# Performance work log

Hardware: AMD Instinct MI355X
Metric: run time of the kernel (lower is better)

The kernel has to match this reference:

```python
import jax, jax.numpy as jnp
import numpy as np

T, B, E, H = 2048, 2, 1024, 16
HD = E // H
EPS = 1e-5


def setup_inputs() -> dict:
    key = jax.random.key(0)
    k1, k2, k3 = jax.random.split(key, 3)
    bound_in = float(np.sqrt(6.0 / (3 * E + E)))   # xavier_uniform for [3E,E]
    bound_out = float(np.sqrt(6.0 / (E + E)))      # xavier_uniform for [E,E]
    return {
        "query": jax.random.normal(k1, (T, B, E), dtype=jnp.float32),
        "gamma": jnp.ones((E,), dtype=jnp.float32),
        "beta": jnp.zeros((E,), dtype=jnp.float32),
        "in_proj_weight": jax.random.uniform(k2, (3 * E, E), jnp.float32, -bound_in, bound_in),
        "out_proj_weight": jax.random.uniform(k3, (E, E), jnp.float32, -bound_out, bound_out),
    }


def reference(query, gamma, beta, in_proj_weight, out_proj_weight):
    # LayerNorm over channel dim
    mean = jnp.mean(query, axis=-1, keepdims=True)
    var = jnp.mean(jnp.square(query - mean), axis=-1, keepdims=True)
    ln = (query - mean) * jax.lax.rsqrt(var + EPS) * gamma + beta  # [T,B,E]

    # Fused QKV projection (no bias): qkv = ln @ W^T, W: [3E, E]
    qkv = jnp.einsum("tbe,fe->tbf", ln, in_proj_weight)  # [T,B,3E]
    q, k, v = jnp.split(qkv, 3, axis=-1)
    q = q.reshape(T, B, H, HD) * (HD ** -0.5)
    k = k.reshape(T, B, H, HD)
    v = v.reshape(T, B, H, HD)

    # Attention: scores [B,H,T,T]
    scores = jnp.einsum("tbhd,sbhd->bhts", q, k)
    attn = jax.nn.softmax(scores, axis=-1)
    ctx = jnp.einsum("bhts,sbhd->tbhd", attn, v).reshape(T, B, E)

    # Output projection + residual add (dropout prob = 0)
    out = jnp.einsum("tbe,fe->tbf", ctx, out_proj_weight)
    return query + out
```

## Files before the change

### kernel.cpp

```cpp
#include <hip/hip_runtime.h>
#include <hip/hip_bf16.h>
#include <math.h>

#define T_DIM 2048
#define B_DIM 2
#define E_DIM 1024
#define H_DIM 16
#define HD_DIM 64
#define M_DIM (T_DIM * B_DIM)
#define BH_DIM (B_DIM * H_DIM)

using bf16x8 = __attribute__((ext_vector_type(8))) __bf16;
using u16x8  = __attribute__((ext_vector_type(8))) unsigned short;
using u16x4  = __attribute__((ext_vector_type(4))) unsigned short;
using f32x4  = __attribute__((ext_vector_type(4))) float;

static __device__ __forceinline__ unsigned short f2bf(float f) {
  unsigned u = __builtin_bit_cast(unsigned, f);
  u += 0x7fff + ((u >> 16) & 1);
  return (unsigned short)(u >> 16);
}

__device__ __forceinline__ void gload_lds16(const void* g, void* l) {
  __builtin_amdgcn_global_load_lds(
      (const __attribute__((address_space(1))) unsigned int*)g,
      (__attribute__((address_space(3))) unsigned int*)l, 16, 0, 0);
}

__global__ __launch_bounds__(256) void cast_bf16_kernel(
    const float* __restrict__ in, unsigned short* __restrict__ out, int n4) {
  int i = blockIdx.x * 256 + threadIdx.x;
  if (i >= n4) return;
  float4 v = ((const float4*)in)[i];
  ushort4 o;
  o.x = f2bf(v.x); o.y = f2bf(v.y); o.z = f2bf(v.z); o.w = f2bf(v.w);
  ((ushort4*)out)[i] = o;
}

__global__ __launch_bounds__(256) void ln_kernel(
    const float* __restrict__ q, const float* __restrict__ gamma,
    const float* __restrict__ beta, unsigned short* __restrict__ out) {
  int row = blockIdx.x;
  int tid = threadIdx.x;
  const float4* qr = (const float4*)(q + (size_t)row * E_DIM);
  float4 x = qr[tid];
  float s  = x.x + x.y + x.z + x.w;
  float ss = x.x * x.x + x.y * x.y + x.z * x.z + x.w * x.w;
#pragma unroll
  for (int off = 32; off >= 1; off >>= 1) {
    s  += __shfl_xor(s, off, 64);
    ss += __shfl_xor(ss, off, 64);
  }
  __shared__ float red[8];
  int wid = tid >> 6, lane = tid & 63;
  if (lane == 0) { red[wid] = s; red[4 + wid] = ss; }
  __syncthreads();
  s  = red[0] + red[1] + red[2] + red[3];
  ss = red[4] + red[5] + red[6] + red[7];
  float mean = s * (1.0f / E_DIM);
  float var  = ss * (1.0f / E_DIM) - mean * mean;
  float rstd = rsqrtf(var + 1e-5f);
  float4 g4 = ((const float4*)gamma)[tid];
  float4 b4 = ((const float4*)beta)[tid];
  ushort4 o;
  o.x = f2bf((x.x - mean) * rstd * g4.x + b4.x);
  o.y = f2bf((x.y - mean) * rstd * g4.y + b4.y);
  o.z = f2bf((x.z - mean) * rstd * g4.z + b4.z);
  o.w = f2bf((x.w - mean) * rstd * g4.w + b4.w);
  ((ushort4*)(out + (size_t)row * E_DIM))[tid] = o;
}

template <int MODE>
__global__ __launch_bounds__(256) void gemm_bt_kernel(
    const unsigned short* __restrict__ A, const unsigned short* __restrict__ Bw,
    const float* __restrict__ resid, unsigned short* __restrict__ out_qkv,
    float* __restrict__ out_f, int Kv, int Nv) {
  __shared__ alignas(16) unsigned short lA[128 * 32];
  __shared__ alignas(16) unsigned short lB[128 * 32];
  int tid = threadIdx.x;
  int wid = tid >> 6, lane = tid & 63;
  int wm = wid >> 1, wn = wid & 1;
  int g = lane >> 4, lr = lane & 15;
  int m0 = blockIdx.y * 128, n0 = blockIdx.x * 128;
  f32x4 acc[4][4] = {};

  for (int k0 = 0; k0 < Kv; k0 += 32) {
#pragma unroll
    for (int c = 0; c < 2; ++c) {
      int f16 = c * 256 + tid;
      int row = f16 >> 2, col8 = (f16 & 3) << 3;
      gload_lds16(A  + (size_t)(m0 + row) * Kv + k0 + col8,
                  lA + (size_t)(c * 256 + wid * 64) * 8);
      gload_lds16(Bw + (size_t)(n0 + row) * Kv + k0 + col8,
                  lB + (size_t)(c * 256 + wid * 64) * 8);
    }
    __syncthreads();
    bf16x8 af[4], bfr[4];
#pragma unroll
    for (int r = 0; r < 4; ++r) {
      af[r]  = *(const bf16x8*)(lA + (wm * 64 + r * 16 + lr) * 32 + g * 8);
      bfr[r] = *(const bf16x8*)(lB + (wn * 64 + r * 16 + lr) * 32 + g * 8);
    }
#pragma unroll
    for (int mr = 0; mr < 4; ++mr)
#pragma unroll
      for (int nr = 0; nr < 4; ++nr)
        acc[mr][nr] = __builtin_amdgcn_mfma_f32_16x16x32_bf16(
            af[mr], bfr[nr], acc[mr][nr], 0, 0, 0);
    __syncthreads();
  }

#pragma unroll
  for (int mr = 0; mr < 4; ++mr) {
#pragma unroll
    for (int nr = 0; nr < 4; ++nr) {
#pragma unroll
      for (int r = 0; r < 4; ++r) {
        int grow = m0 + wm * 64 + mr * 16 + g * 4 + r;
        int gcol = n0 + wn * 64 + nr * 16 + lr;
        float v = acc[mr][nr][r];
        if (MODE == 0) {
          int which = gcol >> 10, rem = gcol & 1023;
          int h = rem >> 6, d = rem & 63;
          int t = grow >> 1, b = grow & 1;
          out_qkv[(size_t)which * (BH_DIM * T_DIM * HD_DIM) +
                  ((size_t)(b * H_DIM + h) * T_DIM + t) * HD_DIM + d] = f2bf(v);
        } else {
          size_t idx = (size_t)grow * Nv + gcol;
          out_f[idx] = resid[idx] + v;
        }
      }
    }
  }
}

__global__ __launch_bounds__(256) void transpose_v_kernel(
    const unsigned short* __restrict__ vb, unsigned short* __restrict__ vt) {
  __shared__ alignas(16) unsigned short tl[64 * 72];
  int tid = threadIdx.x;
  int bh = blockIdx.y, t0 = blockIdx.x * 64;
  const unsigned short* src = vb + ((size_t)bh * T_DIM + t0) * HD_DIM;
#pragma unroll
  for (int e = 0; e < 2; ++e) {
    int i8 = e * 256 + tid;
    int r = i8 >> 3;
    int c = (i8 & 7) * 8;
    int hsh = (r ^ (r >> 3)) & 7;
    bf16x8 v = *(const bf16x8*)(src + (size_t)r * HD_DIM + c);
    *(bf16x8*)(tl + r * 72 + (c ^ (hsh << 3))) = v;
  }
  __syncthreads();
  unsigned short* dst = vt + (size_t)bh * HD_DIM * T_DIM + t0;
#pragma unroll
  for (int e = 0; e < 2; ++e) {
    int i8 = e * 256 + tid;
    int d = i8 >> 3;
    int tc = (i8 & 7) * 8;
    u16x8 o;
#pragma unroll
    for (int j = 0; j < 8; ++j) {
      int p = tc + j;
      int r = ((p & 3) << 4) | (p >> 2);
      int hsh = (r ^ (r >> 3)) & 7;
      o[j] = tl[r * 72 + (d ^ (hsh << 3))];
    }
    *(u16x8*)(dst + (size_t)d * T_DIM + tc) = o;
  }
}

__global__ __launch_bounds__(256) void attn_kernel(
    const unsigned short* __restrict__ qb, const unsigned short* __restrict__ kb,
    const unsigned short* __restrict__ vt, unsigned short* __restrict__ ctx) {
  __shared__ alignas(16) unsigned short lK[3][64 * 64];
  __shared__ alignas(16) unsigned short lV[3][64 * 64];
  __shared__ alignas(16) unsigned short lP[4][32 * 72];
  int tid = threadIdx.x;
  int wid = tid >> 6, lane = tid & 63;
  int g = lane >> 4, lr = lane & 15;
  int bh = blockIdx.y;
  int b = bh >> 4, h = bh & 15;
  int qt = blockIdx.x;
  const size_t koff = (size_t)bh * T_DIM * HD_DIM;
  const size_t voff = (size_t)bh * HD_DIM * T_DIM;

  int srow = tid >> 3;
  int gch  = (tid & 7) ^ (srow & 7);
  const unsigned short* ks0 = kb + koff + (size_t)srow * HD_DIM + gch * 8;
  const unsigned short* vs0 = vt + voff + (size_t)srow * T_DIM + gch * 8;

#define STAGE_TILE(buf, kofs, vofs)                                            \
  do {                                                                         \
    gload_lds16(ks0 + (kofs),                 lK[buf] + wid * 512);            \
    gload_lds16(ks0 + (kofs) + 32 * HD_DIM,   lK[buf] + 2048 + wid * 512);     \
    gload_lds16(vs0 + (vofs),                 lV[buf] + wid * 512);            \
    gload_lds16(vs0 + (vofs) + (size_t)32 * T_DIM, lV[buf] + 2048 + wid * 512);\
  } while (0)

  bf16x8 qf[2][2];
  {
    const float QS = 0.125f * 1.44269504f;
#pragma unroll
    for (int qa = 0; qa < 2; ++qa) {
      int qrow = qt * 128 + wid * 32 + qa * 16 + lr;
#pragma unroll
      for (int ks = 0; ks < 2; ++ks) {
        bf16x8 raw = *(const bf16x8*)(qb + koff + (size_t)qrow * HD_DIM + ks * 32 + g * 8);
#pragma unroll
        for (int j = 0; j < 8; ++j) qf[qa][ks][j] = (__bf16)((float)raw[j] * QS);
      }
    }
  }

  bf16x8 onesf;
#pragma unroll
  for (int j = 0; j < 8; ++j) onesf[j] = (__bf16)1.0f;

  f32x4 accO[2][4] = {};
  f32x4 accS[2] = {};

  const int NT = T_DIM / 64;
  STAGE_TILE(0, 0, 0);

#define PROCESS(BUF, NBUF, TT, LAST)                                           \
  do {                                                                         \
    if (!(LAST)) {                                                             \
      size_t s1 = (size_t)((TT) + 1) * 64;                                     \
      STAGE_TILE(NBUF, s1 * HD_DIM, s1);                                       \
      asm volatile("s_waitcnt vmcnt(4)" ::: "memory");                         \
    } else {                                                                   \
      asm volatile("s_waitcnt vmcnt(0)" ::: "memory");                         \
    }                                                                          \
    __builtin_amdgcn_s_barrier();                                              \
    __builtin_amdgcn_sched_barrier(0);                                         \
    const unsigned short* Kc = lK[BUF];                                        \
    const unsigned short* Vc = lV[BUF];                                        \
    f32x4 s4[2][4];                                                            \
    __builtin_amdgcn_s_setprio(1);                                             \
    _Pragma("unroll")                                                          \
    for (int cf = 0; cf < 4; ++cf) {                                           \
      int row = cf * 16 + lr;                                                  \
      int sw = (row & 7) << 3;                                                 \
      bf16x8 k0 = *(const bf16x8*)(Kc + row * 64 + ((g * 8) ^ sw));            \
      bf16x8 k1 = *(const bf16x8*)(Kc + row * 64 + ((32 + g * 8) ^ sw));       \
      _Pragma("unroll")                                                        \
      for (int qa = 0; qa < 2; ++qa) {                                         \
        f32x4 s = {-8.0f, -8.0f, -8.0f, -8.0f};                                \
        s = __builtin_amdgcn_mfma_f32_16x16x32_bf16(qf[qa][0], k0, s, 0, 0, 0);\
        s = __builtin_amdgcn_mfma_f32_16x16x32_bf16(qf[qa][1], k1, s, 0, 0, 0);\
        s4[qa][cf] = s;                                                        \
      }                                                                        \
    }                                                                          \
    __builtin_amdgcn_s_setprio(0);                                             \
    _Pragma("unroll")                                                          \
    for (int qa = 0; qa < 2; ++qa)                                             \
      _Pragma("unroll")                                                        \
      for (int r = 0; r < 4; ++r) {                                            \
        u16x4 pk;                                                              \
        _Pragma("unroll")                                                      \
        for (int cf = 0; cf < 4; ++cf)                                         \
          pk[cf] = __builtin_bit_cast(unsigned short,                          \
                     (__bf16)__builtin_amdgcn_exp2f(s4[qa][cf][r]));           \
        *(u16x4*)(&lP[wid][(qa * 16 + g * 4 + r) * 72 + lr * 4]) = pk;         \
      }                                                                        \
    __builtin_amdgcn_s_setprio(1);                                             \
    _Pragma("unroll")                                                          \
    for (int ks = 0; ks < 2; ++ks) {                                           \
      bf16x8 pf[2];                                                            \
      _Pragma("unroll")                                                        \
      for (int qa = 0; qa < 2; ++qa) {                                         \
        pf[qa] = *(const bf16x8*)(&lP[wid][(qa * 16 + lr) * 72 + ks * 32 + g * 8]); \
        accS[qa] = __builtin_amdgcn_mfma_f32_16x16x32_bf16(pf[qa], onesf, accS[qa], 0, 0, 0); \
      }                                                                        \
      _Pragma("unroll")                                                        \
      for (int df = 0; df < 4; ++df) {                                         \
        int row = df * 16 + lr;                                                \
        int sw = (row & 7) << 3;                                               \
        bf16x8 vf = *(const bf16x8*)(Vc + row * 64 + ((ks * 32 + g * 8) ^ sw));\
        _Pragma("unroll")                                                      \
        for (int qa = 0; qa < 2; ++qa)                                         \
          accO[qa][df] = __builtin_amdgcn_mfma_f32_16x16x32_bf16(pf[qa], vf, accO[qa][df], 0, 0, 0); \
      }                                                                        \
    }                                                                          \
    __builtin_amdgcn_s_setprio(0);                                             \
  } while (0)

  for (int t3 = 0; t3 < 30; t3 += 3) {
    PROCESS(0, 1, t3 + 0, false);
    PROCESS(1, 2, t3 + 1, false);
    PROCESS(2, 0, t3 + 2, false);
  }
  PROCESS(0, 1, 30, false);
  PROCESS(1, 2, 31, true);
#undef PROCESS
#undef STAGE_TILE

#pragma unroll
  for (int qa = 0; qa < 2; ++qa) {
    float invl[4];
#pragma unroll
    for (int r = 0; r < 4; ++r) invl[r] = 1.0f / accS[qa][r];
#pragma unroll
    for (int df = 0; df < 4; ++df) {
#pragma unroll
      for (int r = 0; r < 4; ++r) {
        int t = qt * 128 + wid * 32 + qa * 16 + g * 4 + r;
        int col = h * HD_DIM + df * 16 + lr;
        float o = accO[qa][df][r] * invl[r];
        ctx[((size_t)t * B_DIM + b) * E_DIM + col] = f2bf(o);
      }
    }
  }
}

extern "C" void kernel_launch(void* const* d_in, const int* in_sizes, int n_in,
                              void* d_out, int out_size, void* d_ws, size_t ws_size,
                              hipStream_t stream) {
  const float* query = (const float*)d_in[0];
  const float* gamma = (const float*)d_in[1];
  const float* beta  = (const float*)d_in[2];
  const float* w_in  = (const float*)d_in[3];
  const float* w_out = (const float*)d_in[4];
  float* out = (float*)d_out;

  unsigned short* ws    = (unsigned short*)d_ws;
  unsigned short* ln    = ws;
  unsigned short* winb  = ln + (size_t)M_DIM * E_DIM;
  unsigned short* woutb = winb + (size_t)3 * E_DIM * E_DIM;
  unsigned short* qkv   = woutb + (size_t)E_DIM * E_DIM;

  unsigned short* qbuf = qkv;
  unsigned short* kbuf = qkv + (size_t)BH_DIM * T_DIM * HD_DIM;
  unsigned short* vbuf = kbuf + (size_t)BH_DIM * T_DIM * HD_DIM;
  unsigned short* vtb  = ln;
  unsigned short* ctx  = vbuf;

  cast_bf16_kernel<<<dim3(3072), dim3(256), 0, stream>>>(w_in, winb, 3 * E_DIM * E_DIM / 4);
  cast_bf16_kernel<<<dim3(1024), dim3(256), 0, stream>>>(w_out, woutb, E_DIM * E_DIM / 4);
  ln_kernel<<<dim3(M_DIM), dim3(256), 0, stream>>>(query, gamma, beta, ln);
  gemm_bt_kernel<0><<<dim3(3 * E_DIM / 128, M_DIM / 128), dim3(256), 0, stream>>>(
      ln, winb, nullptr, qkv, nullptr, E_DIM, 3 * E_DIM);
  transpose_v_kernel<<<dim3(T_DIM / 64, BH_DIM), dim3(256), 0, stream>>>(vbuf, vtb);
  attn_kernel<<<dim3(T_DIM / 128, BH_DIM), dim3(256), 0, stream>>>(qbuf, kbuf, vtb, ctx);
  gemm_bt_kernel<1><<<dim3(E_DIM / 128, M_DIM / 128), dim3(256), 0, stream>>>(
      ctx, woutb, query, nullptr, out, E_DIM, E_DIM);
}
```

Before: 137.7 us.

## Keep P in registers via transposed MFMA, remap blocks, retile out-proj GEMM

Several changes land together. The attention kernel swaps the MFMA operand order so the exponentiated P fragments stay in registers instead of going through an LDS round-trip, with the V transpose permutation changed to match. Attention blocks are remapped so heads spread across XCDs, and the epilogue stages context through LDS for 16-byte coalesced stores. The two weight casts are merged into one launch, and the output projection uses 128x64 tiles to put more blocks on the CUs. Risks include correctness coupling between the V permutation and the fragment layout, and a smaller per-block tile in the out-proj GEMM.

```diff
diff --git a/kernel.cpp b/kernel.cpp
--- a/kernel.cpp
+++ b/kernel.cpp
@@ -27,14 +27,18 @@
       (__attribute__((address_space(3))) unsigned int*)l, 16, 0, 0);
 }
 
-__global__ __launch_bounds__(256) void cast_bf16_kernel(
-    const float* __restrict__ in, unsigned short* __restrict__ out, int n4) {
+__global__ __launch_bounds__(256) void cast2_kernel(
+    const float* __restrict__ in1, unsigned short* __restrict__ out1, int n1,
+    const float* __restrict__ in2, unsigned short* __restrict__ out2, int n2) {
   int i = blockIdx.x * 256 + threadIdx.x;
-  if (i >= n4) return;
-  float4 v = ((const float4*)in)[i];
+  const float* in; unsigned short* out; int idx;
+  if (i < n1) { in = in1; out = out1; idx = i; }
+  else if (i < n1 + n2) { in = in2; out = out2; idx = i - n1; }
+  else return;
+  float4 v = ((const float4*)in)[idx];
   ushort4 o;
   o.x = f2bf(v.x); o.y = f2bf(v.y); o.z = f2bf(v.z); o.w = f2bf(v.w);
-  ((ushort4*)out)[i] = o;
+  ((ushort4*)out)[idx] = o;
 }
 
 __global__ __launch_bounds__(256) void ln_kernel(
@@ -70,11 +74,9 @@
   ((ushort4*)(out + (size_t)row * E_DIM))[tid] = o;
 }
 
-template <int MODE>
-__global__ __launch_bounds__(256) void gemm_bt_kernel(
+__global__ __launch_bounds__(256) void gemm0_kernel(
     const unsigned short* __restrict__ A, const unsigned short* __restrict__ Bw,
-    const float* __restrict__ resid, unsigned short* __restrict__ out_qkv,
-    float* __restrict__ out_f, int Kv, int Nv) {
+    unsigned short* __restrict__ out_qkv) {
   __shared__ alignas(16) unsigned short lA[128 * 32];
   __shared__ alignas(16) unsigned short lB[128 * 32];
   int tid = threadIdx.x;
@@ -84,14 +86,14 @@
   int m0 = blockIdx.y * 128, n0 = blockIdx.x * 128;
   f32x4 acc[4][4] = {};
 
-  for (int k0 = 0; k0 < Kv; k0 += 32) {
+  for (int k0 = 0; k0 < E_DIM; k0 += 32) {
 #pragma unroll
     for (int c = 0; c < 2; ++c) {
       int f16 = c * 256 + tid;
       int row = f16 >> 2, col8 = (f16 & 3) << 3;
-      gload_lds16(A  + (size_t)(m0 + row) * Kv + k0 + col8,
+      gload_lds16(A  + (size_t)(m0 + row) * E_DIM + k0 + col8,
                   lA + (size_t)(c * 256 + wid * 64) * 8);
-      gload_lds16(Bw + (size_t)(n0 + row) * Kv + k0 + col8,
+      gload_lds16(Bw + (size_t)(n0 + row) * E_DIM + k0 + col8,
                   lB + (size_t)(c * 256 + wid * 64) * 8);
     }
     __syncthreads();
@@ -118,17 +120,68 @@
       for (int r = 0; r < 4; ++r) {
         int grow = m0 + wm * 64 + mr * 16 + g * 4 + r;
         int gcol = n0 + wn * 64 + nr * 16 + lr;
-        float v = acc[mr][nr][r];
-        if (MODE == 0) {
-          int which = gcol >> 10, rem = gcol & 1023;
-          int h = rem >> 6, d = rem & 63;
-          int t = grow >> 1, b = grow & 1;
-          out_qkv[(size_t)which * (BH_DIM * T_DIM * HD_DIM) +
-                  ((size_t)(b * H_DIM + h) * T_DIM + t) * HD_DIM + d] = f2bf(v);
-        } else {
-          size_t idx = (size_t)grow * Nv + gcol;
-          out_f[idx] = resid[idx] + v;
-        }
+        int which = gcol >> 10, rem = gcol & 1023;
+        int h = rem >> 6, d = rem & 63;
+        int t = grow >> 1, b = grow & 1;
+        out_qkv[(size_t)which * (BH_DIM * T_DIM * HD_DIM) +
+                ((size_t)(b * H_DIM + h) * T_DIM + t) * HD_DIM + d] =
+            f2bf(acc[mr][nr][r]);
+      }
+    }
+  }
+}
+
+__global__ __launch_bounds__(256) void gemm1_kernel(
+    const unsigned short* __restrict__ A, const unsigned short* __restrict__ Bw,
+    const float* __restrict__ resid, float* __restrict__ out) {
+  __shared__ alignas(16) unsigned short lA[128 * 32];
+  __shared__ alignas(16) unsigned short lB[64 * 32];
+  int tid = threadIdx.x;
+  int wid = tid >> 6, lane = tid & 63;
+  int g = lane >> 4, lr = lane & 15;
+  int m0 = blockIdx.y * 128, n0 = blockIdx.x * 64;
+  f32x4 acc[2][4] = {};
+
+  for (int k0 = 0; k0 < E_DIM; k0 += 32) {
+#pragma unroll
+    for (int c = 0; c < 2; ++c) {
+      int f16 = c * 256 + tid;
+      int row = f16 >> 2, col8 = (f16 & 3) << 3;
+      gload_lds16(A + (size_t)(m0 + row) * E_DIM + k0 + col8,
+                  lA + (size_t)(c * 256 + wid * 64) * 8);
+    }
+    {
+      int row = tid >> 2, col8 = (tid & 3) << 3;
+      gload_lds16(Bw + (size_t)(n0 + row) * E_DIM + k0 + col8,
+                  lB + (size_t)(wid * 64) * 8);
+    }
+    __syncthreads();
+    bf16x8 af[2], bfr[4];
+#pragma unroll
+    for (int r = 0; r < 2; ++r)
+      af[r] = *(const bf16x8*)(lA + (wid * 32 + r * 16 + lr) * 32 + g * 8);
+#pragma unroll
+    for (int r = 0; r < 4; ++r)
+      bfr[r] = *(const bf16x8*)(lB + (r * 16 + lr) * 32 + g * 8);
+#pragma unroll
+    for (int mr = 0; mr < 2; ++mr)
+#pragma unroll
+      for (int nr = 0; nr < 4; ++nr)
+        acc[mr][nr] = __builtin_amdgcn_mfma_f32_16x16x32_bf16(
+            af[mr], bfr[nr], acc[mr][nr], 0, 0, 0);
+    __syncthreads();
+  }
+
+#pragma unroll
+  for (int mr = 0; mr < 2; ++mr) {
+#pragma unroll
+    for (int nr = 0; nr < 4; ++nr) {
+#pragma unroll
+      for (int r = 0; r < 4; ++r) {
+        int grow = m0 + wid * 32 + mr * 16 + g * 4 + r;
+        int gcol = n0 + nr * 16 + lr;
+        size_t idx = (size_t)grow * E_DIM + gcol;
+        out[idx] = resid[idx] + acc[mr][nr][r];
       }
     }
   }
@@ -160,7 +213,8 @@
 #pragma unroll
     for (int j = 0; j < 8; ++j) {
       int p = tc + j;
-      int r = ((p & 3) << 4) | (p >> 2);
+      int ks = p >> 5, gg = (p >> 3) & 3, jl = p & 7;
+      int r = (ks * 2 + (jl >> 2)) * 16 + gg * 4 + (jl & 3);
       int hsh = (r ^ (r >> 3)) & 7;
       o[j] = tl[r * 72 + (d ^ (hsh << 3))];
     }
@@ -173,13 +227,14 @@
     const unsigned short* __restrict__ vt, unsigned short* __restrict__ ctx) {
   __shared__ alignas(16) unsigned short lK[3][64 * 64];
   __shared__ alignas(16) unsigned short lV[3][64 * 64];
-  __shared__ alignas(16) unsigned short lP[4][32 * 72];
   int tid = threadIdx.x;
   int wid = tid >> 6, lane = tid & 63;
   int g = lane >> 4, lr = lane & 15;
-  int bh = blockIdx.y;
+  int f = blockIdx.x;
+  int xcd = f & 7, rest = f >> 3;
+  int bh = xcd + 8 * (rest & 3);
+  int qt = rest >> 2;
   int b = bh >> 4, h = bh & 15;
-  int qt = blockIdx.x;
   const size_t koff = (size_t)bh * T_DIM * HD_DIM;
   const size_t voff = (size_t)bh * HD_DIM * T_DIM;
 
@@ -245,32 +300,26 @@
       _Pragma("unroll")                                                        \
       for (int qa = 0; qa < 2; ++qa) {                                         \
         f32x4 s = {-8.0f, -8.0f, -8.0f, -8.0f};                                \
-        s = __builtin_amdgcn_mfma_f32_16x16x32_bf16(qf[qa][0], k0, s, 0, 0, 0);\
-        s = __builtin_amdgcn_mfma_f32_16x16x32_bf16(qf[qa][1], k1, s, 0, 0, 0);\
+        s = __builtin_amdgcn_mfma_f32_16x16x32_bf16(k0, qf[qa][0], s, 0, 0, 0);\
+        s = __builtin_amdgcn_mfma_f32_16x16x32_bf16(k1, qf[qa][1], s, 0, 0, 0);\
         s4[qa][cf] = s;                                                        \
       }                                                                        \
     }                                                                          \
     __builtin_amdgcn_s_setprio(0);                                             \
+    bf16x8 pf[2][2];                                                           \
     _Pragma("unroll")                                                          \
     for (int qa = 0; qa < 2; ++qa)                                             \
       _Pragma("unroll")                                                        \
-      for (int r = 0; r < 4; ++r) {                                            \
-        u16x4 pk;                                                              \
-        _Pragma("unroll")                                                      \
-        for (int cf = 0; cf < 4; ++cf)                                         \
-          pk[cf] = __builtin_bit_cast(unsigned short,                          \
-                     (__bf16)__builtin_amdgcn_exp2f(s4[qa][cf][r]));           \
-        *(u16x4*)(&lP[wid][(qa * 16 + g * 4 + r) * 72 + lr * 4]) = pk;         \
+      for (int j = 0; j < 8; ++j) {                                            \
+        pf[qa][0][j] = (__bf16)__builtin_amdgcn_exp2f(s4[qa][(j >> 2)][j & 3]);\
+        pf[qa][1][j] = (__bf16)__builtin_amdgcn_exp2f(s4[qa][2 + (j >> 2)][j & 3]);\
       }                                                                        \
     __builtin_amdgcn_s_setprio(1);                                             \
     _Pragma("unroll")                                                          \
     for (int ks = 0; ks < 2; ++ks) {                                           \
-      bf16x8 pf[2];                                                            \
       _Pragma("unroll")                                                        \
-      for (int qa = 0; qa < 2; ++qa) {                                         \
-        pf[qa] = *(const bf16x8*)(&lP[wid][(qa * 16 + lr) * 72 + ks * 32 + g * 8]); \
-        accS[qa] = __builtin_amdgcn_mfma_f32_16x16x32_bf16(pf[qa], onesf, accS[qa], 0, 0, 0); \
-      }                                                                        \
+      for (int qa = 0; qa < 2; ++qa)                                           \
+        accS[qa] = __builtin_amdgcn_mfma_f32_16x16x32_bf16(onesf, pf[qa][ks], accS[qa], 0, 0, 0); \
       _Pragma("unroll")                                                        \
       for (int df = 0; df < 4; ++df) {                                         \
         int row = df * 16 + lr;                                                \
@@ -278,7 +327,7 @@
         bf16x8 vf = *(const bf16x8*)(Vc + row * 64 + ((ks * 32 + g * 8) ^ sw));\
         _Pragma("unroll")                                                      \
         for (int qa = 0; qa < 2; ++qa)                                         \
-          accO[qa][df] = __builtin_amdgcn_mfma_f32_16x16x32_bf16(pf[qa], vf, accO[qa][df], 0, 0, 0); \
+          accO[qa][df] = __builtin_amdgcn_mfma_f32_16x16x32_bf16(vf, pf[qa][ks], accO[qa][df], 0, 0, 0); \
       }                                                                        \
     }                                                                          \
     __builtin_amdgcn_s_setprio(0);                                             \
@@ -294,21 +343,27 @@
 #undef PROCESS
 #undef STAGE_TILE
 
-#pragma unroll
-  for (int qa = 0; qa < 2; ++qa) {
-    float invl[4];
-#pragma unroll
-    for (int r = 0; r < 4; ++r) invl[r] = 1.0f / accS[qa][r];
-#pragma unroll
-    for (int df = 0; df < 4; ++df) {
-#pragma unroll
-      for (int r = 0; r < 4; ++r) {
-        int t = qt * 128 + wid * 32 + qa * 16 + g * 4 + r;
-        int col = h * HD_DIM + df * 16 + lr;
-        float o = accO[qa][df][r] * invl[r];
-        ctx[((size_t)t * B_DIM + b) * E_DIM + col] = f2bf(o);
-      }
-    }
+  __syncthreads();
+  unsigned short* sc = (unsigned short*)lK + wid * (32 * 72);
+  float invl[2];
+  invl[0] = 1.0f / accS[0][0];
+  invl[1] = 1.0f / accS[1][0];
+#pragma unroll
+  for (int qa = 0; qa < 2; ++qa)
+#pragma unroll
+    for (int df = 0; df < 4; ++df)
+#pragma unroll
+      for (int r = 0; r < 4; ++r)
+        sc[(qa * 16 + lr) * 72 + df * 16 + g * 4 + r] =
+            f2bf(accO[qa][df][r] * invl[qa]);
+  __syncthreads();
+#pragma unroll
+  for (int i = 0; i < 4; ++i) {
+    int idx = i * 64 + lane;
+    int row = idx >> 3, ch = idx & 7;
+    u16x8 v8 = *(const u16x8*)(sc + row * 72 + ch * 8);
+    int t = qt * 128 + wid * 32 + row;
+    *(u16x8*)(&ctx[((size_t)t * B_DIM + b) * E_DIM + h * HD_DIM + ch * 8]) = v8;
   }
 }
 
@@ -334,13 +389,13 @@
   unsigned short* vtb  = ln;
   unsigned short* ctx  = vbuf;
 
-  cast_bf16_kernel<<<dim3(3072), dim3(256), 0, stream>>>(w_in, winb, 3 * E_DIM * E_DIM / 4);
-  cast_bf16_kernel<<<dim3(1024), dim3(256), 0, stream>>>(w_out, woutb, E_DIM * E_DIM / 4);
+  cast2_kernel<<<dim3(4096), dim3(256), 0, stream>>>(
+      w_in, winb, 3 * E_DIM * E_DIM / 4, w_out, woutb, E_DIM * E_DIM / 4);
   ln_kernel<<<dim3(M_DIM), dim3(256), 0, stream>>>(query, gamma, beta, ln);
-  gemm_bt_kernel<0><<<dim3(3 * E_DIM / 128, M_DIM / 128), dim3(256), 0, stream>>>(
-      ln, winb, nullptr, qkv, nullptr, E_DIM, 3 * E_DIM);
+  gemm0_kernel<<<dim3(3 * E_DIM / 128, M_DIM / 128), dim3(256), 0, stream>>>(
+      ln, winb, qkv);
   transpose_v_kernel<<<dim3(T_DIM / 64, BH_DIM), dim3(256), 0, stream>>>(vbuf, vtb);
-  attn_kernel<<<dim3(T_DIM / 128, BH_DIM), dim3(256), 0, stream>>>(qbuf, kbuf, vtb, ctx);
-  gemm_bt_kernel<1><<<dim3(E_DIM / 128, M_DIM / 128), dim3(256), 0, stream>>>(
-      ctx, woutb, query, nullptr, out, E_DIM, E_DIM);
-}
+  attn_kernel<<<dim3(512), dim3(256), 0, stream>>>(qbuf, kbuf, vtb, ctx);
+  gemm1_kernel<<<dim3(E_DIM / 64, M_DIM / 128), dim3(256), 0, stream>>>(
+      ctx, woutb, query, out);
+}
```

New measurement: 122.3 us. -11.2%, faster.
